# Kernel optimization log

Hardware: AMD Instinct MI355X
Metric: run time of the kernel (lower is better)

Reference implementation:

```python
import jax, jax.numpy as jnp
import numpy as np

N_NODE, K_PATH, L_PATH = 50000, 8, 6
D_NODE, D_PATH = 64, 128
N_EDGE = 1600000


def setup_inputs() -> dict:
    key = jax.random.key(0)
    k1, k2, k3, k4, k5 = jax.random.split(key, 5)
    feat = jax.random.normal(k1, (N_NODE, D_NODE), dtype=jnp.float32)
    weight = jax.random.uniform(k2, (N_EDGE,), dtype=jnp.float32)
    W = jax.random.normal(k3, (D_PATH, D_NODE * (L_PATH - 1)), dtype=jnp.float32) * 0.05
    paths = jax.random.randint(k4, (N_NODE, K_PATH, L_PATH), 0, N_NODE + 1, dtype=jnp.int64)
    edge_ids = jax.random.randint(k5, (N_NODE, K_PATH, L_PATH - 1), 0, N_EDGE, dtype=jnp.int64)
    return {"feat": feat, "weight": weight, "W": W, "paths": paths, "edge_ids": edge_ids}


def reference(feat, weight, W, paths, edge_ids):
    # Pad node features with one zero row: index n_node -> zeros (matches torch cat trick).
    feat_pad = jnp.concatenate([feat, jnp.zeros((1, feat.shape[1]), dtype=feat.dtype)], axis=0)
    # Gather: [n_node, k_path, l_path, d_node]
    path_feat = feat_pad[paths]
    # Edge weights: [n_node, k_path, l_path-1, 1]
    eweight = weight[edge_ids][..., None]
    # Weighted combine of consecutive nodes along the path.
    combined = path_feat[..., : L_PATH - 1, :] + eweight * path_feat[..., 1:L_PATH, :]
    # Flatten last two dims -> [n_node, k_path, d_node*(l_path-1)], then project.
    flat = combined.reshape(combined.shape[0], combined.shape[1], -1)
    return jnp.einsum("nkf,df->nkd", flat, W)
```

## Files before the change

### kernel.cpp

```cpp
#include <hip/hip_runtime.h>
#include <hip/hip_bf16.h>

typedef __bf16 bf16x8 __attribute__((ext_vector_type(8)));
typedef float f32x4 __attribute__((ext_vector_type(4)));

#define N_NODE 50000
#define KPATH 8
#define LPATH 6
#define DNODE 64
#define DPATH 128
#define KDIM 320
#define NPAIR (N_NODE * KPATH)
#define M_BLK 32
#define NBLK (NPAIR / M_BLK)
#define ROW_BYTES 640
#define WF_BYTES 81920
#define FEATB_BYTES (N_NODE * DNODE * 2)

__device__ __forceinline__ int swz(int row, int bytecol) {
    return row * ROW_BYTES + (bytecol ^ ((row & 7) << 4));
}

__global__ void wfrag_prep(const float* __restrict__ W, __bf16* __restrict__ wf) {
    int t = blockIdx.x * 256 + threadIdx.x;
    if (t >= 8 * 10 * 64 * 8) return;
    int j    = t & 7;
    int lane = (t >> 3) & 63;
    int ks   = (t >> 9) % 10;
    int nt   = t / 5120;
    int k = ks * 32 + (lane >> 4) * 8 + j;
    int n = nt * 16 + (lane & 15);
    wf[t] = (__bf16)W[n * KDIM + k];
}

__global__ void feat_prep(const float* __restrict__ f, __bf16* __restrict__ fb) {
    int t = blockIdx.x * 256 + threadIdx.x;
    if (t >= N_NODE * DNODE / 8) return;
    float4 a = ((const float4*)f)[t * 2];
    float4 b = ((const float4*)f)[t * 2 + 1];
    union { bf16x8 v; __bf16 e[8]; } u;
    u.e[0] = (__bf16)a.x; u.e[1] = (__bf16)a.y; u.e[2] = (__bf16)a.z; u.e[3] = (__bf16)a.w;
    u.e[4] = (__bf16)b.x; u.e[5] = (__bf16)b.y; u.e[6] = (__bf16)b.z; u.e[7] = (__bf16)b.w;
    ((bf16x8*)fb)[t] = u.v;
}

template <bool BF16FEAT>
__global__ __launch_bounds__(256) void path_gemm(
    const void*  __restrict__ featv,
    const float* __restrict__ weight,
    const int*   __restrict__ paths,
    const int*   __restrict__ eids,
    const __bf16* __restrict__ wf,
    float* __restrict__ out)
{
    __shared__ bf16x8 AsVec[M_BLK * ROW_BYTES / 16];
    char* asb = (char*)AsVec;

    const int  t  = threadIdx.x;
    const long p0 = (long)blockIdx.x * M_BLK;

    {
        const int  r  = t >> 3;
        const int  s  = t & 7;
        const int  d0 = s * 8;
        const int  lr = r & 7;
        const long p  = p0 + r;

        int pv = 0;
        if (s < LPATH) pv = __builtin_nontemporal_load(paths + p * LPATH + s);
        float wv = 0.f;
        if (s < LPATH - 1) {
            int ev = __builtin_nontemporal_load(eids + p * (LPATH - 1) + s);
            wv = weight[ev];
        }

        int idx[LPATH];
#pragma unroll
        for (int l = 0; l < LPATH; ++l) idx[l] = __shfl(pv, lr * 8 + l, 64);
        float ew[LPATH - 1];
#pragma unroll
        for (int l = 0; l < LPATH - 1; ++l) ew[l] = __shfl(wv, lr * 8 + l, 64);

        float x[8];
#pragma unroll
        for (int l = 0; l < LPATH; ++l) {
            float y[8];
            const int id = idx[l];
            if (id >= N_NODE) {
#pragma unroll
                for (int i = 0; i < 8; ++i) y[i] = 0.f;
            } else if (BF16FEAT) {
                union { bf16x8 v; __bf16 e[8]; } u;
                u.v = *(const bf16x8*)((const __bf16*)featv + (long)id * DNODE + d0);
#pragma unroll
                for (int i = 0; i < 8; ++i) y[i] = (float)u.e[i];
            } else {
                const float4* sp = (const float4*)((const float*)featv + (long)id * DNODE + d0);
                *(float4*)&y[0] = sp[0];
                *(float4*)&y[4] = sp[1];
            }
            if (l > 0) {
                union { bf16x8 v; __bf16 e[8]; } u;
#pragma unroll
                for (int i = 0; i < 8; ++i) u.e[i] = (__bf16)(x[i] + ew[l - 1] * y[i]);
                *(bf16x8*)(asb + swz(r, (l - 1) * 128 + s * 16)) = u.v;
            }
#pragma unroll
            for (int i = 0; i < 8; ++i) x[i] = y[i];
        }
    }
    __syncthreads();

    const int wave = t >> 6;
    const int lane = t & 63;
    const int lrow = lane & 15;
    const int h    = lane >> 4;

    f32x4 acc[2][2];
#pragma unroll
    for (int mt = 0; mt < 2; ++mt)
#pragma unroll
        for (int nt = 0; nt < 2; ++nt)
            acc[mt][nt] = (f32x4){0.f, 0.f, 0.f, 0.f};

#pragma unroll
    for (int ks = 0; ks < 10; ++ks) {
        bf16x8 b0 = *(const bf16x8*)(wf + (((wave * 2 + 0) * 10 + ks) * 64 + lane) * 8);
        bf16x8 b1 = *(const bf16x8*)(wf + (((wave * 2 + 1) * 10 + ks) * 64 + lane) * 8);
#pragma unroll
        for (int mt = 0; mt < 2; ++mt) {
            bf16x8 a = *(const bf16x8*)(asb + swz(mt * 16 + lrow, ks * 64 + h * 16));
            acc[mt][0] = __builtin_amdgcn_mfma_f32_16x16x32_bf16(a, b0, acc[mt][0], 0, 0, 0);
            acc[mt][1] = __builtin_amdgcn_mfma_f32_16x16x32_bf16(a, b1, acc[mt][1], 0, 0, 0);
        }
    }

    const int rbase = h * 4;
#pragma unroll
    for (int mt = 0; mt < 2; ++mt) {
#pragma unroll
        for (int nt = 0; nt < 2; ++nt) {
#pragma unroll
            for (int q = 0; q < 4; ++q) {
                long row = p0 + mt * 16 + rbase + q;
                int  col = wave * 32 + nt * 16 + lrow;
                __builtin_nontemporal_store(acc[mt][nt][q], &out[row * DPATH + col]);
            }
        }
    }
}

extern "C" void kernel_launch(void* const* d_in, const int* in_sizes, int n_in,
                              void* d_out, int out_size, void* d_ws, size_t ws_size,
                              hipStream_t stream) {
    const float* feat   = (const float*)d_in[0];
    const float* weight = (const float*)d_in[1];
    const float* W      = (const float*)d_in[2];
    const int*   paths  = (const int*)d_in[3];
    const int*   eids   = (const int*)d_in[4];
    float* out = (float*)d_out;
    __bf16* wf = (__bf16*)d_ws;
    __bf16* featb = (__bf16*)((char*)d_ws + WF_BYTES);

    wfrag_prep<<<160, 256, 0, stream>>>(W, wf);

    if (ws_size >= (size_t)WF_BYTES + FEATB_BYTES) {
        feat_prep<<<(N_NODE * DNODE / 8 + 255) / 256, 256, 0, stream>>>(feat, featb);
        path_gemm<true><<<NBLK, 256, 0, stream>>>(featb, weight, paths, eids, wf, out);
    } else {
        path_gemm<false><<<NBLK, 256, 0, stream>>>(feat, weight, paths, eids, wf, out);
    }
}
```

Measured before the change: 123.6 us.

## Make path_gemm persistent with register-resident W fragments and bf16 edge weights

Converts the GEMM kernel to a persistent grid of 1024 blocks that loop over tiles. The W fragments are loaded into registers once per block instead of once per tile, and the LDS tile is double-buffered to allow overlap across iterations. Edge weights are also pre-converted to bf16 in a new prep kernel, which halves the bytes of the random weight gather but adds an extra launch and more rounding. Holding 40 bf16x8 values in registers raises register pressure under launch_bounds(256,4), and the persistent loop relies on a single __syncthreads per tile.

```diff
diff --git a/kernel.cpp b/kernel.cpp
--- a/kernel.cpp
+++ b/kernel.cpp
@@ -10,12 +10,15 @@
 #define DNODE 64
 #define DPATH 128
 #define KDIM 320
+#define N_EDGE 1600000
 #define NPAIR (N_NODE * KPATH)
 #define M_BLK 32
-#define NBLK (NPAIR / M_BLK)
+#define NTILE (NPAIR / M_BLK)
+#define GRID 1024
 #define ROW_BYTES 640
 #define WF_BYTES 81920
 #define FEATB_BYTES (N_NODE * DNODE * 2)
+#define EWB_BYTES (N_EDGE * 2)
 
 __device__ __forceinline__ int swz(int row, int bytecol) {
     return row * ROW_BYTES + (bytecol ^ ((row & 7) << 4));
@@ -33,9 +36,9 @@
     wf[t] = (__bf16)W[n * KDIM + k];
 }
 
-__global__ void feat_prep(const float* __restrict__ f, __bf16* __restrict__ fb) {
+__global__ void bf16_prep(const float* __restrict__ f, __bf16* __restrict__ fb, int n8) {
     int t = blockIdx.x * 256 + threadIdx.x;
-    if (t >= N_NODE * DNODE / 8) return;
+    if (t >= n8) return;
     float4 a = ((const float4*)f)[t * 2];
     float4 b = ((const float4*)f)[t * 2 + 1];
     union { bf16x8 v; __bf16 e[8]; } u;
@@ -44,107 +47,117 @@
     ((bf16x8*)fb)[t] = u.v;
 }
 
-template <bool BF16FEAT>
-__global__ __launch_bounds__(256) void path_gemm(
+template <bool PREP>
+__global__ __launch_bounds__(256, 4) void path_gemm(
     const void*  __restrict__ featv,
-    const float* __restrict__ weight,
+    const void*  __restrict__ weightv,
     const int*   __restrict__ paths,
     const int*   __restrict__ eids,
     const __bf16* __restrict__ wf,
     float* __restrict__ out)
 {
-    __shared__ bf16x8 AsVec[M_BLK * ROW_BYTES / 16];
-    char* asb = (char*)AsVec;
+    __shared__ bf16x8 AsVec[2][M_BLK * ROW_BYTES / 16];
 
-    const int  t  = threadIdx.x;
-    const long p0 = (long)blockIdx.x * M_BLK;
+    const int t    = threadIdx.x;
+    const int wave = t >> 6;
+    const int lane = t & 63;
 
-    {
-        const int  r  = t >> 3;
-        const int  s  = t & 7;
-        const int  d0 = s * 8;
-        const int  lr = r & 7;
-        const long p  = p0 + r;
+    bf16x8 breg[10][2];
+#pragma unroll
+    for (int ks = 0; ks < 10; ++ks)
+#pragma unroll
+        for (int nt = 0; nt < 2; ++nt)
+            breg[ks][nt] = *(const bf16x8*)(wf + (((wave * 2 + nt) * 10 + ks) * 64 + lane) * 8);
 
-        int pv = 0;
-        if (s < LPATH) pv = __builtin_nontemporal_load(paths + p * LPATH + s);
-        float wv = 0.f;
-        if (s < LPATH - 1) {
-            int ev = __builtin_nontemporal_load(eids + p * (LPATH - 1) + s);
-            wv = weight[ev];
+    const int r  = t >> 3;
+    const int s  = t & 7;
+    const int d0 = s * 8;
+    const int lr = (t >> 3) & 7;
+
+    const int lrow = lane & 15;
+    const int h    = lane >> 4;
+    const int rbase = h * 4;
+
+    int it = 0;
+    for (int tile = blockIdx.x; tile < NTILE; tile += GRID, ++it) {
+        char* asb = (char*)AsVec[it & 1];
+        const long p0 = (long)tile * M_BLK;
+
+        {
+            const long p = p0 + r;
+            int pv = 0;
+            if (s < LPATH) pv = __builtin_nontemporal_load(paths + p * LPATH + s);
+            float wv = 0.f;
+            if (s < LPATH - 1) {
+                int ev = __builtin_nontemporal_load(eids + p * (LPATH - 1) + s);
+                wv = PREP ? (float)((const __bf16*)weightv)[ev]
+                          : ((const float*)weightv)[ev];
+            }
+
+            int idx[LPATH];
+#pragma unroll
+            for (int l = 0; l < LPATH; ++l) idx[l] = __shfl(pv, lr * 8 + l, 64);
+            float ew[LPATH - 1];
+#pragma unroll
+            for (int l = 0; l < LPATH - 1; ++l) ew[l] = __shfl(wv, lr * 8 + l, 64);
+
+            float x[8];
+#pragma unroll
+            for (int l = 0; l < LPATH; ++l) {
+                float y[8];
+                const int id = idx[l];
+                if (id >= N_NODE) {
+#pragma unroll
+                    for (int i = 0; i < 8; ++i) y[i] = 0.f;
+                } else if (PREP) {
+                    union { bf16x8 v; __bf16 e[8]; } u;
+                    u.v = *(const bf16x8*)((const __bf16*)featv + (long)id * DNODE + d0);
+#pragma unroll
+                    for (int i = 0; i < 8; ++i) y[i] = (float)u.e[i];
+                } else {
+                    const float4* sp = (const float4*)((const float*)featv + (long)id * DNODE + d0);
+                    *(float4*)&y[0] = sp[0];
+                    *(float4*)&y[4] = sp[1];
+                }
+                if (l > 0) {
+                    union { bf16x8 v; __bf16 e[8]; } u;
+#pragma unroll
+                    for (int i = 0; i < 8; ++i) u.e[i] = (__bf16)(x[i] + ew[l - 1] * y[i]);
+                    *(bf16x8*)(asb + swz(r, (l - 1) * 128 + s * 16)) = u.v;
+                }
+#pragma unroll
+                for (int i = 0; i < 8; ++i) x[i] = y[i];
+            }
+        }
+        __syncthreads();
+
+        f32x4 acc[2][2];
+#pragma unroll
+        for (int mt = 0; mt < 2; ++mt)
+#pragma unroll
+            for (int nt = 0; nt < 2; ++nt)
+                acc[mt][nt] = (f32x4){0.f, 0.f, 0.f, 0.f};
+
+#pragma unroll
+        for (int ks = 0; ks < 10; ++ks) {
+#pragma unroll
+            for (int mt = 0; mt < 2; ++mt) {
+                bf16x8 a = *(const bf16x8*)(asb + swz(mt * 16 + lrow, ks * 64 + h * 16));
+                acc[mt][0] = __builtin_amdgcn_mfma_f32_16x16x32_bf16(a, breg[ks][0], acc[mt][0], 0, 0, 0);
+                acc[mt][1] = __builtin_amdgcn_mfma_f32_16x16x32_bf16(a, breg[ks][1], acc[mt][1], 0, 0, 0);
+            }
         }
 
-        int idx[LPATH];
-#pragma unroll
-        for (int l = 0; l < LPATH; ++l) idx[l] = __shfl(pv, lr * 8 + l, 64);
-        float ew[LPATH - 1];
-#pragma unroll
-        for (int l = 0; l < LPATH - 1; ++l) ew[l] = __shfl(wv, lr * 8 + l, 64);
-
-        float x[8];
-#pragma unroll
-        for (int l = 0; l < LPATH; ++l) {
-            float y[8];
-            const int id = idx[l];
-            if (id >= N_NODE) {
-#pragma unroll
-                for (int i = 0; i < 8; ++i) y[i] = 0.f;
-            } else if (BF16FEAT) {
-                union { bf16x8 v; __bf16 e[8]; } u;
-                u.v = *(const bf16x8*)((const __bf16*)featv + (long)id * DNODE + d0);
-#pragma unroll
-                for (int i = 0; i < 8; ++i) y[i] = (float)u.e[i];
-            } else {
-                const float4* sp = (const float4*)((const float*)featv + (long)id * DNODE + d0);
-                *(float4*)&y[0] = sp[0];
-                *(float4*)&y[4] = sp[1];
-            }
-            if (l > 0) {
-                union { bf16x8 v; __bf16 e[8]; } u;
-#pragma unroll
-                for (int i = 0; i < 8; ++i) u.e[i] = (__bf16)(x[i] + ew[l - 1] * y[i]);
-                *(bf16x8*)(asb + swz(r, (l - 1) * 128 + s * 16)) = u.v;
-            }
-#pragma unroll
-            for (int i = 0; i < 8; ++i) x[i] = y[i];
-        }
-    }
-    __syncthreads();
-
-    const int wave = t >> 6;
-    const int lane = t & 63;
-    const int lrow = lane & 15;
-    const int h    = lane >> 4;
-
-    f32x4 acc[2][2];
-#pragma unroll
-    for (int mt = 0; mt < 2; ++mt)
-#pragma unroll
-        for (int nt = 0; nt < 2; ++nt)
-            acc[mt][nt] = (f32x4){0.f, 0.f, 0.f, 0.f};
-
-#pragma unroll
-    for (int ks = 0; ks < 10; ++ks) {
-        bf16x8 b0 = *(const bf16x8*)(wf + (((wave * 2 + 0) * 10 + ks) * 64 + lane) * 8);
-        bf16x8 b1 = *(const bf16x8*)(wf + (((wave * 2 + 1) * 10 + ks) * 64 + lane) * 8);
 #pragma unroll
         for (int mt = 0; mt < 2; ++mt) {
-            bf16x8 a = *(const bf16x8*)(asb + swz(mt * 16 + lrow, ks * 64 + h * 16));
-            acc[mt][0] = __builtin_amdgcn_mfma_f32_16x16x32_bf16(a, b0, acc[mt][0], 0, 0, 0);
-            acc[mt][1] = __builtin_amdgcn_mfma_f32_16x16x32_bf16(a, b1, acc[mt][1], 0, 0, 0);
-        }
-    }
-
-    const int rbase = h * 4;
 #pragma unroll
-    for (int mt = 0; mt < 2; ++mt) {
+            for (int nt = 0; nt < 2; ++nt) {
 #pragma unroll
-        for (int nt = 0; nt < 2; ++nt) {
-#pragma unroll
-            for (int q = 0; q < 4; ++q) {
-                long row = p0 + mt * 16 + rbase + q;
-                int  col = wave * 32 + nt * 16 + lrow;
-                __builtin_nontemporal_store(acc[mt][nt][q], &out[row * DPATH + col]);
+                for (int q = 0; q < 4; ++q) {
+                    long row = p0 + mt * 16 + rbase + q;
+                    int  col = wave * 32 + nt * 16 + lrow;
+                    __builtin_nontemporal_store(acc[mt][nt][q], &out[row * DPATH + col]);
+                }
             }
         }
     }
@@ -159,15 +172,18 @@
     const int*   paths  = (const int*)d_in[3];
     const int*   eids   = (const int*)d_in[4];
     float* out = (float*)d_out;
-    __bf16* wf = (__bf16*)d_ws;
+
+    __bf16* wf    = (__bf16*)d_ws;
     __bf16* featb = (__bf16*)((char*)d_ws + WF_BYTES);
+    __bf16* ewb   = (__bf16*)((char*)d_ws + WF_BYTES + FEATB_BYTES);
 
     wfrag_prep<<<160, 256, 0, stream>>>(W, wf);
 
-    if (ws_size >= (size_t)WF_BYTES + FEATB_BYTES) {
-        feat_prep<<<(N_NODE * DNODE / 8 + 255) / 256, 256, 0, stream>>>(feat, featb);
-        path_gemm<true><<<NBLK, 256, 0, stream>>>(featb, weight, paths, eids, wf, out);
+    if (ws_size >= (size_t)WF_BYTES + FEATB_BYTES + EWB_BYTES) {
+        bf16_prep<<<(N_NODE * DNODE / 8 + 255) / 256, 256, 0, stream>>>(feat, featb, N_NODE * DNODE / 8);
+        bf16_prep<<<(N_EDGE / 8 + 255) / 256, 256, 0, stream>>>(weight, ewb, N_EDGE / 8);
+        path_gemm<true><<<GRID, 256, 0, stream>>>(featb, ewb, paths, eids, wf, out);
     } else {
-        path_gemm<false><<<NBLK, 256, 0, stream>>>(feat, weight, paths, eids, wf, out);
+        path_gemm<false><<<GRID, 256, 0, stream>>>(feat, weight, paths, eids, wf, out);
     }
 }
```

New measurement: 158.7 us. +28.3%, slower.
